# Performance work log

Measured on AMD Instinct MI355X. Metric: run time of the kernel, lower is better.

## Reference

```python
import jax, jax.numpy as jnp
import numpy as np

EPS = 1e-6
NORM_FACTOR = 1000.0  # self.normalization_factor, aggregation 'sum'

# ---- Lorentz manifold (curvature -1, hyperboloid <x,x>_L = -1) ----

def _linner(x, y):
    # Lorentz inner product, keepdim on last axis
    return -x[..., :1] * y[..., :1] + jnp.sum(x[..., 1:] * y[..., 1:], axis=-1, keepdims=True)

def _proj_tan0(u):
    return jnp.concatenate([jnp.zeros_like(u[..., :1]), u[..., 1:]], axis=-1)

def _expmap0(u):
    sp = u[..., 1:]
    n = jnp.sqrt(jnp.clip(jnp.sum(sp * sp, axis=-1, keepdims=True), EPS))
    return jnp.concatenate([jnp.cosh(n), jnp.sinh(n) / n * sp], axis=-1)

def _logmap0(x):
    x0 = jnp.clip(x[..., :1], 1.0 + EPS)
    d = jnp.arccosh(x0)
    sp = x[..., 1:] * (d / jnp.sqrt(x0 * x0 - 1.0))
    return jnp.concatenate([jnp.zeros_like(x0), sp], axis=-1)

def _dist(x, y):
    return jnp.arccosh(jnp.clip(-_linner(x, y), 1.0 + EPS))

def _logmap(x, y):
    alpha = jnp.clip(-_linner(x, y), 1.0 + EPS)
    u = y - alpha * x                      # y + <x,y>_L x
    return jnp.arccosh(alpha) * u / jnp.sqrt(alpha * alpha - 1.0)

def _expmap(x, u):
    n = jnp.sqrt(jnp.clip(_linner(u, u), EPS))
    return jnp.cosh(n) * x + jnp.sinh(n) / n * u

def _proju(x, u):
    return u + _linner(x, u) * x

def _transp0(y, v):
    # parallel transport from origin o=(1,0,...,0) to y
    coef = _linner(y, v) / (1.0 + y[..., :1])
    oy = jnp.concatenate([y[..., :1] + 1.0, y[..., 1:]], axis=-1)
    return v + coef * oy

def _layernorm(x, g, b, eps=1e-5):
    m = jnp.mean(x, axis=-1, keepdims=True)
    v = jnp.mean((x - m) ** 2, axis=-1, keepdims=True)
    return (x - m) / jnp.sqrt(v + eps) * g + b


def setup_inputs() -> dict:
    N, E, D, ED = 10000, 320000, 128, 2
    key = jax.random.key(0)
    ks = jax.random.split(key, 10)
    # nodes on the hyperboloid: expmap0 of a small tangent vector
    h_tan = 0.02 * jax.random.normal(ks[0], (N, D), dtype=jnp.float32)
    h = _expmap0(_proj_tan0(h_tan))
    edge_attr = jax.random.normal(ks[1], (E, ED), dtype=jnp.float32)
    row = jax.random.randint(ks[2], (E,), 0, N, dtype=jnp.int32)
    col = jax.random.randint(ks[3], (E,), 0, N, dtype=jnp.int32)
    node_mask = jnp.ones((N, 1), dtype=jnp.float32)
    edge_mask = jnp.ones((E, 1), dtype=jnp.float32)
    s = 1.0 / np.sqrt(D)
    W = s * jax.random.normal(ks[4], (D, D), dtype=jnp.float32)
    bias = 0.0 * jax.random.normal(ks[5], (1, D), dtype=jnp.float32)  # init.constant_(bias, 0)
    att_in = 2 * D + ED + 1  # x_row, x_col, edge_attr + geodesic
    att_w1 = (1.0 / np.sqrt(att_in)) * jax.random.normal(ks[6], (att_in, D), dtype=jnp.float32)
    att_b1 = jnp.zeros((D,), dtype=jnp.float32)
    att_w2 = s * jax.random.normal(ks[7], (D, 1), dtype=jnp.float32)
    att_b2 = jnp.zeros((1,), dtype=jnp.float32)
    ln_gamma = jnp.ones((D - 1,), dtype=jnp.float32)
    ln_beta = jnp.zeros((D - 1,), dtype=jnp.float32)
    return {"h": h, "edge_attr": edge_attr, "row": row, "col": col,
            "node_mask": node_mask, "edge_mask": edge_mask, "W": W, "bias": bias,
            "att_w1": att_w1, "att_b1": att_b1, "att_w2": att_w2, "att_b2": att_b2,
            "ln_gamma": ln_gamma, "ln_beta": ln_beta}


def reference(h, edge_attr, row, col, node_mask, edge_mask, W, bias,
              att_w1, att_b1, att_w2, att_b2, ln_gamma, ln_beta):
    N = h.shape[0]
    # ---- HypLinear ----
    xt = _logmap0(h) @ W                  # Linear(in,out,bias=False)
    x = _expmap0(_proj_tan0(xt))
    b = _transp0(x, _proj_tan0(bias))
    x = _expmap(x, b)
    # ---- HypAgg ----
    x_tan = _logmap0(x)
    xr, xc = x[row], x[col]
    geo = _dist(xr, xc)                   # [E,1]
    att_in = jnp.concatenate([x_tan[row], x_tan[col], edge_attr, geo], axis=-1)
    hid = jax.nn.silu(att_in @ att_w1 + att_b1)
    att = jax.nn.sigmoid(hid @ att_w2 + att_b2) * edge_mask   # [E,1]
    loc = _logmap(xr, xc)                 # [E,D]
    agg = jax.ops.segment_sum(loc * att, row, num_segments=N) / NORM_FACTOR
    x = _expmap(x, _proju(x, agg))
    # ---- HNorm (Lorentz: LN on spatial components only) ----
    ht = _logmap0(x)
    sp = _layernorm(ht[..., 1:], ln_gamma, ln_beta)
    x = _expmap0(jnp.concatenate([ht[..., :1], sp], axis=-1))
    # ---- HypAct (manifold_out = Lorentz as well) ----
    xt = _proj_tan0(jax.nn.silu(_logmap0(x)))
    return _expmap0(xt)
```

## Files before the change

### kernel.cpp

```cpp
#include <hip/hip_runtime.h>
#include <math.h>

#define D 128
#define NPB 8
#define EPS1 (1.0f + 1e-6f)

__device__ __forceinline__ float dpp_rsum16(float v) {
    v += __int_as_float(__builtin_amdgcn_update_dpp(
        0, __float_as_int(v), 0x121, 0xf, 0xf, true));
    v += __int_as_float(__builtin_amdgcn_update_dpp(
        0, __float_as_int(v), 0x122, 0xf, 0xf, true));
    v += __int_as_float(__builtin_amdgcn_update_dpp(
        0, __float_as_int(v), 0x124, 0xf, 0xf, true));
    v += __int_as_float(__builtin_amdgcn_update_dpp(
        0, __float_as_int(v), 0x128, 0xf, 0xf, true));
    return v;
}

__device__ __forceinline__ float facosh(float a) {
    return __logf(a + sqrtf(fmaxf(a * a - 1.0f, 0.0f)));
}

__device__ __forceinline__ void unpack8(const float4& a, const float4& b,
                                        float* d) {
    d[0] = a.x; d[1] = a.y; d[2] = a.z; d[3] = a.w;
    d[4] = b.x; d[5] = b.y; d[6] = b.z; d[7] = b.w;
}

__device__ __forceinline__ void bsumH(float* v, float (*wred)[4], int lane,
                                      int wid, int kp) {
    __syncthreads();
#pragma unroll
    for (int o = 32; o; o >>= 1)
#pragma unroll
        for (int nl = 0; nl < 4; nl++) v[nl] += __shfl_xor(v[nl], o, 64);
    if (lane == 0)
#pragma unroll
        for (int nl = 0; nl < 4; nl++) wred[wid][nl] = v[nl];
    __syncthreads();
#pragma unroll
    for (int nl = 0; nl < 4; nl++)
        v[nl] = wred[2 * kp][nl] + wred[2 * kp + 1][nl];
}

__global__ __launch_bounds__(256) void node_pre8(
    const float* __restrict__ h, const float* __restrict__ W,
    const float* __restrict__ bias, const float* __restrict__ att_w1,
    const float* __restrict__ att_b1, float* __restrict__ XQ,
    float* __restrict__ P_out, const int* __restrict__ row,
    int* __restrict__ cnt, int N, int E) {
    int i0 = blockIdx.x * NPB;
    int tid = threadIdx.x;
    int j = tid & 127, kp = tid >> 7;
    int lane = tid & 63, wid = tid >> 6;
    int nbase = kp * 4;
    __shared__ __align__(16) float t8[NPB][D];
    __shared__ float psumP[2][NPB][D];
    __shared__ float psumQ[2][NPB][D];
    __shared__ float wred[4][4];

    float hj[4];
#pragma unroll
    for (int nl = 0; nl < 4; nl++) {
        int gi = i0 + nbase + nl;
        hj[nl] = (gi < N) ? h[(size_t)gi * D + j] : 0.0f;
        t8[nbase + nl][j] = hj[nl];
    }
    __syncthreads();
    float tj[4];
#pragma unroll
    for (int nl = 0; nl < 4; nl++) {
        float h0 = fmaxf(t8[nbase + nl][0], EPS1);
        float fac = facosh(h0) * rsqrtf(h0 * h0 - 1.0f);
        tj[nl] = (j == 0) ? 0.0f : hj[nl] * fac;
    }
    __syncthreads();
#pragma unroll
    for (int nl = 0; nl < 4; nl++) t8[nbase + nl][j] = tj[nl];
    __syncthreads();

    float xtp[NPB];
#pragma unroll
    for (int n = 0; n < NPB; n++) xtp[n] = 0.0f;
    int kbeg = kp * 64;
    for (int k0 = kbeg; k0 < kbeg + 64; k0 += 4) {
        float w0 = W[(k0 + 0) * D + j], w1 = W[(k0 + 1) * D + j];
        float w2 = W[(k0 + 2) * D + j], w3 = W[(k0 + 3) * D + j];
#pragma unroll
        for (int n = 0; n < NPB; n++) {
            float4 tv = *(const float4*)&t8[n][k0];
            xtp[n] = fmaf(tv.x, w0,
                          fmaf(tv.y, w1, fmaf(tv.z, w2, fmaf(tv.w, w3, xtp[n]))));
        }
    }
#pragma unroll
    for (int n = 0; n < NPB; n++) psumP[kp][n][j] = xtp[n];
    __syncthreads();
    float xt[4];
#pragma unroll
    for (int nl = 0; nl < 4; nl++) {
        int n = nbase + nl;
        xt[nl] = (j == 0) ? 0.0f : (psumP[0][n][j] + psumP[1][n][j]);
    }

    float v4[4];
#pragma unroll
    for (int nl = 0; nl < 4; nl++) v4[nl] = xt[nl] * xt[nl];
    bsumH(v4, wred, lane, wid, kp);
    float xj[4];
#pragma unroll
    for (int nl = 0; nl < 4; nl++) {
        float nn = sqrtf(fmaxf(v4[nl], 1e-6f));
        float e = __expf(nn), ei = __fdividef(1.0f, e);
        float ch = 0.5f * (e + ei), sh = 0.5f * (e - ei);
        xj[nl] = (j == 0) ? ch : __fdividef(sh, nn) * xt[nl];
    }

    float vj = (j == 0) ? 0.0f : bias[j];
#pragma unroll
    for (int nl = 0; nl < 4; nl++) v4[nl] = xj[nl] * vj;
    bsumH(v4, wred, lane, wid, kp);
    __syncthreads();
#pragma unroll
    for (int nl = 0; nl < 4; nl++) t8[nbase + nl][j] = xj[nl];
    __syncthreads();
    float bj[4];
#pragma unroll
    for (int nl = 0; nl < 4; nl++) {
        float X0 = t8[nbase + nl][0];
        float coef = __fdividef(v4[nl], 1.0f + X0);
        bj[nl] = vj + coef * ((j == 0) ? (X0 + 1.0f) : xj[nl]);
    }
#pragma unroll
    for (int nl = 0; nl < 4; nl++)
        v4[nl] = (j == 0) ? -bj[nl] * bj[nl] : bj[nl] * bj[nl];
    bsumH(v4, wred, lane, wid, kp);
    float xnj[4];
#pragma unroll
    for (int nl = 0; nl < 4; nl++) {
        float nb = sqrtf(fmaxf(v4[nl], 1e-6f));
        float e = __expf(nb), ei = __fdividef(1.0f, e);
        float ch = 0.5f * (e + ei), sh = 0.5f * (e - ei);
        xnj[nl] = ch * xj[nl] + __fdividef(sh, nb) * bj[nl];
        int gi = i0 + nbase + nl;
        if (gi < N) XQ[(size_t)gi * 256 + j] = xnj[nl];
    }

    __syncthreads();
#pragma unroll
    for (int nl = 0; nl < 4; nl++) t8[nbase + nl][j] = xnj[nl];
    __syncthreads();
    float xtj[4];
#pragma unroll
    for (int nl = 0; nl < 4; nl++) {
        float Y0 = fmaxf(t8[nbase + nl][0], EPS1);
        float f = facosh(Y0) * rsqrtf(Y0 * Y0 - 1.0f);
        xtj[nl] = (j == 0) ? 0.0f : xnj[nl] * f;
    }
    __syncthreads();
#pragma unroll
    for (int nl = 0; nl < 4; nl++) t8[nbase + nl][j] = xtj[nl];
    __syncthreads();

    float pp[NPB], qq[NPB];
#pragma unroll
    for (int n = 0; n < NPB; n++) {
        pp[n] = 0.0f;
        qq[n] = 0.0f;
    }
    for (int k0 = kbeg; k0 < kbeg + 64; k0 += 4) {
        float a0 = att_w1[(k0 + 0) * D + j], a1 = att_w1[(k0 + 1) * D + j];
        float a2 = att_w1[(k0 + 2) * D + j], a3 = att_w1[(k0 + 3) * D + j];
        float c0 = att_w1[(D + k0 + 0) * D + j], c1 = att_w1[(D + k0 + 1) * D + j];
        float c2 = att_w1[(D + k0 + 2) * D + j], c3 = att_w1[(D + k0 + 3) * D + j];
#pragma unroll
        for (int n = 0; n < NPB; n++) {
            float4 tv = *(const float4*)&t8[n][k0];
            pp[n] = fmaf(tv.x, a0,
                         fmaf(tv.y, a1, fmaf(tv.z, a2, fmaf(tv.w, a3, pp[n]))));
            qq[n] = fmaf(tv.x, c0,
                         fmaf(tv.y, c1, fmaf(tv.z, c2, fmaf(tv.w, c3, qq[n]))));
        }
    }
#pragma unroll
    for (int n = 0; n < NPB; n++) {
        psumP[kp][n][j] = pp[n];
        psumQ[kp][n][j] = qq[n];
    }
    __syncthreads();
    float b1 = att_b1[j];
#pragma unroll
    for (int nl = 0; nl < 4; nl++) {
        int n = nbase + nl;
        int gi = i0 + n;
        if (gi < N) {
            P_out[(size_t)gi * D + j] = psumP[0][n][j] + psumP[1][n][j] + b1;
            XQ[(size_t)gi * 256 + 128 + j] = psumQ[0][n][j] + psumQ[1][n][j];
        }
    }

    int gtid = blockIdx.x * 256 + tid;
    int tot = gridDim.x * 256;
    for (int e2 = gtid; e2 < E; e2 += tot) atomicAdd(&cnt[row[e2]], 1);
}

__global__ __launch_bounds__(1024) void scan_kernel(const int* __restrict__ cnt,
                                                    int* __restrict__ off,
                                                    int* __restrict__ cursor,
                                                    int N) {
    __shared__ int wsum[16];
    __shared__ int carry_s;
    int tid = threadIdx.x, lane = tid & 63, wid = tid >> 6;
    if (tid == 0) carry_s = 0;
    __syncthreads();
    for (int base = 0; base < N; base += 1024) {
        int idx = base + tid;
        int v = (idx < N) ? cnt[idx] : 0;
        int orig = v;
#pragma unroll
        for (int o = 1; o < 64; o <<= 1) {
            int t = __shfl_up(v, o, 64);
            if (lane >= o) v += t;
        }
        if (lane == 63) wsum[wid] = v;
        __syncthreads();
        if (wid == 0 && lane < 16) {
            int w = wsum[lane];
#pragma unroll
            for (int o = 1; o < 16; o <<= 1) {
                int t = __shfl_up(w, o, 64);
                if (lane >= o) w += t;
            }
            wsum[lane] = w;
        }
        __syncthreads();
        int carry = carry_s;
        int wbase = (wid == 0) ? 0 : wsum[wid - 1];
        int excl = carry + wbase + v - orig;
        if (idx < N) {
            off[idx] = excl;
            cursor[idx] = excl;
        }
        __syncthreads();
        if (tid == 1023) carry_s = carry + wsum[15];
        __syncthreads();
    }
}

__global__ void scatter_kernel(const int* __restrict__ row,
                               const int* __restrict__ col,
                               const float* __restrict__ edge_attr,
                               const float* __restrict__ edge_mask,
                               int* __restrict__ cursor,
                               float4* __restrict__ rec, int E) {
    const float2* ea2 = (const float2*)edge_attr;
    for (int e = blockIdx.x * blockDim.x + threadIdx.x; e < E;
         e += gridDim.x * blockDim.x) {
        int r = row[e];
        int pos = atomicAdd(&cursor[r], 1);
        float2 a = ea2[e];
        rec[pos] = make_float4(__int_as_float(col[e]), a.x, a.y, edge_mask[e]);
    }
}

__global__ __launch_bounds__(256) void edge_agg(
    const float* __restrict__ XQ, const float* __restrict__ P,
    const float4* __restrict__ rec, const int* __restrict__ off,
    const int* __restrict__ cnt, const float* __restrict__ w1c,
    const float* __restrict__ att_w2, const float* __restrict__ att_b2,
    const float* __restrict__ gamma, const float* __restrict__ beta,
    float* __restrict__ out, int N) {
    int tid = threadIdx.x, lane = tid & 63;
    int sub = lane & 15, grp = lane >> 4;
    int i = blockIdx.x * 4 + (tid >> 6);
    bool valid = i < N;
    i = min(i, N - 1);
    int j8 = sub * 8, f4 = sub * 2;

    const float4* w4 = (const float4*)w1c;
    const float4* aw4 = (const float4*)att_w2;
    const float4* xq4r = (const float4*)(XQ + (size_t)i * 256);
    const float4* pr4 = (const float4*)(P + (size_t)i * D);
    float xr[8], pr[8], wa[8], wb[8], wg[8], w2v[8];
    unpack8(xq4r[f4], xq4r[f4 + 1], xr);
    unpack8(pr4[f4], pr4[f4 + 1], pr);
    unpack8(w4[f4], w4[f4 + 1], wa);
    unpack8(w4[32 + f4], w4[32 + f4 + 1], wb);
    unpack8(w4[64 + f4], w4[64 + f4 + 1], wg);
    unpack8(aw4[f4], aw4[f4 + 1], w2v);
    float b2 = att_b2[0];
    float xr0s = (sub == 0) ? -xr[0] : xr[0];

    float acc[8];
#pragma unroll
    for (int u = 0; u < 8; u++) acc[u] = 0.0f;

    int s = off[i], m = valid ? cnt[i] : 0;
    int clen = (m + 3) >> 2;
    int k0 = grp * clen;
    int len = min(m, k0 + clen) - k0;

    auto compute = [&](const float4& rc, const float4& g0, const float4& g1,
                       const float4& g2, const float4& g3, bool act) {
        float xc[8], qc[8];
        unpack8(g0, g1, xc);
        unpack8(g2, g3, qc);
        float lin = xr0s * xc[0];
#pragma unroll
        for (int u = 1; u < 8; u++) lin = fmaf(xr[u], xc[u], lin);
        lin = dpp_rsum16(lin);
        float alpha = fmaxf(-lin, EPS1);
        float a2m = fmaxf(fmaf(alpha, alpha, -1.0f), 1e-12f);
        float rden = rsqrtf(a2m);
        float geo = __logf(fmaf(a2m, rden, alpha));
        float lp = 0.0f;
#pragma unroll
        for (int u = 0; u < 8; u++) {
            float hv = pr[u] + qc[u] +
                       fmaf(rc.y, wa[u], fmaf(rc.z, wb[u], geo * wg[u]));
            float sig = __fdividef(1.0f, 1.0f + __expf(-hv));
            lp = fmaf(hv * sig, w2v[u], lp);
        }
        lp = dpp_rsum16(lp);
        float w = act ? rc.w : 0.0f;
        float att = w * __fdividef(1.0f, 1.0f + __expf(-(lp + b2)));
        float scale = att * geo * rden * 1e-3f;
#pragma unroll
        for (int u = 0; u < 8; u++)
            acc[u] = fmaf(scale, fmaf(-alpha, xr[u], xc[u]), acc[u]);
    };

    float4 rcA = make_float4(__int_as_float(0), 0.0f, 0.0f, 0.0f), rcB;
    if (len > 0) rcA = rec[s + k0];
    const float4* pA =
        (const float4*)(XQ + (size_t)__float_as_int(rcA.x) * 256);
    float4 gA0 = pA[f4], gA1 = pA[f4 + 1], gA2 = pA[32 + f4],
           gA3 = pA[32 + f4 + 1];
    float4 gB0, gB1, gB2, gB3;

    for (int t = 0; t < clen; t += 2) {
        rcB = rcA;
        if (t + 1 < len) rcB = rec[s + k0 + t + 1];
        const float4* pB =
            (const float4*)(XQ + (size_t)__float_as_int(rcB.x) * 256);
        gB0 = pB[f4]; gB1 = pB[f4 + 1]; gB2 = pB[32 + f4]; gB3 = pB[32 + f4 + 1];
        compute(rcA, gA0, gA1, gA2, gA3, t < len);
        rcA = rcB;
        if (t + 2 < len) rcA = rec[s + k0 + t + 2];
        const float4* pN =
            (const float4*)(XQ + (size_t)__float_as_int(rcA.x) * 256);
        gA0 = pN[f4]; gA1 = pN[f4 + 1]; gA2 = pN[32 + f4]; gA3 = pN[32 + f4 + 1];
        compute(rcB, gB0, gB1, gB2, gB3, t + 1 < len);
    }

#pragma unroll
    for (int u = 0; u < 8; u++) {
        acc[u] += __shfl_xor(acc[u], 16, 64);
        acc[u] += __shfl_xor(acc[u], 32, 64);
    }

    float lxa_p = (sub == 0) ? -xr[0] * acc[0] : xr[0] * acc[0];
#pragma unroll
    for (int u = 1; u < 8; u++) lxa_p = fmaf(xr[u], acc[u], lxa_p);
    float lxa = dpp_rsum16(lxa_p);
    float uj[8];
#pragma unroll
    for (int u = 0; u < 8; u++) uj[u] = fmaf(lxa, xr[u], acc[u]);
    float luu_p = (sub == 0) ? -uj[0] * uj[0] : uj[0] * uj[0];
#pragma unroll
    for (int u = 1; u < 8; u++) luu_p = fmaf(uj[u], uj[u], luu_p);
    float luu = dpp_rsum16(luu_p);
    float nn = sqrtf(fmaxf(luu, 1e-6f));
    float e = __expf(nn), ei = __fdividef(1.0f, e);
    float ch = 0.5f * (e + ei), shv = __fdividef(0.5f * (e - ei), nn);
    float xn[8];
#pragma unroll
    for (int u = 0; u < 8; u++) xn[u] = ch * xr[u] + shv * uj[u];
    float X0 = __shfl(xn[0], lane & 48, 64);
    X0 = fmaxf(X0, EPS1);
    float fc = facosh(X0) * rsqrtf(X0 * X0 - 1.0f);
    float ht[8];
#pragma unroll
    for (int u = 0; u < 8; u++) ht[u] = xn[u] * fc;
    if (sub == 0) ht[0] = 0.0f;
    float mp = 0.0f;
#pragma unroll
    for (int u = 0; u < 8; u++) mp += ht[u];
    float mean = dpp_rsum16(mp) * (1.0f / 127.0f);
    float diff[8];
#pragma unroll
    for (int u = 0; u < 8; u++) diff[u] = ht[u] - mean;
    if (sub == 0) diff[0] = 0.0f;
    float vp = 0.0f;
#pragma unroll
    for (int u = 0; u < 8; u++) vp = fmaf(diff[u], diff[u], vp);
    float var = dpp_rsum16(vp) * (1.0f / 127.0f);
    float rstd = rsqrtf(var + 1e-5f);
    float sp[8];
#pragma unroll
    for (int u = 0; u < 8; u++) {
        int j = j8 + u;
        sp[u] = (j > 0) ? fmaf(diff[u] * rstd, gamma[j - 1], beta[j - 1]) : 0.0f;
    }
    float n2p = 0.0f;
#pragma unroll
    for (int u = 0; u < 8; u++) n2p = fmaf(sp[u], sp[u], n2p);
    float n2 = sqrtf(fmaxf(dpp_rsum16(n2p), 1e-6f));
    e = __expf(n2);
    ei = __fdividef(1.0f, e);
    float y0 = 0.5f * (e + ei), sh2 = __fdividef(0.5f * (e - ei), n2);
    float yj[8];
#pragma unroll
    for (int u = 0; u < 8; u++) yj[u] = sh2 * sp[u];
    if (sub == 0) yj[0] = y0;
    float y0c = fmaxf(y0, EPS1);
    float f3 = facosh(y0c) * rsqrtf(y0c * y0c - 1.0f);
    float sj[8];
#pragma unroll
    for (int u = 0; u < 8; u++) {
        float lj = yj[u] * f3;
        sj[u] = __fdividef(lj, 1.0f + __expf(-lj));
    }
    if (sub == 0) sj[0] = 0.0f;
    float n3p = 0.0f;
#pragma unroll
    for (int u = 0; u < 8; u++) n3p = fmaf(sj[u], sj[u], n3p);
    float n3 = sqrtf(fmaxf(dpp_rsum16(n3p), 1e-6f));
    e = __expf(n3);
    ei = __fdividef(1.0f, e);
    float o0 = 0.5f * (e + ei), sh3 = __fdividef(0.5f * (e - ei), n3);
    float ov[8];
#pragma unroll
    for (int u = 0; u < 8; u++) ov[u] = sh3 * sj[u];
    if (sub == 0) ov[0] = o0;
    if (valid && grp == 0) {
        float4* o4 = (float4*)(out + (size_t)i * D);
        o4[f4] = make_float4(ov[0], ov[1], ov[2], ov[3]);
        o4[f4 + 1] = make_float4(ov[4], ov[5], ov[6], ov[7]);
    }
}

extern "C" void kernel_launch(void* const* d_in, const int* in_sizes, int n_in,
                              void* d_out, int out_size, void* d_ws,
                              size_t ws_size, hipStream_t stream) {
    const float* h = (const float*)d_in[0];
    const float* edge_attr = (const float*)d_in[1];
    const int* row = (const int*)d_in[2];
    const int* col = (const int*)d_in[3];
    const float* edge_mask = (const float*)d_in[5];
    const float* W = (const float*)d_in[6];
    const float* bias = (const float*)d_in[7];
    const float* att_w1 = (const float*)d_in[8];
    const float* att_b1 = (const float*)d_in[9];
    const float* att_w2 = (const float*)d_in[10];
    const float* att_b2 = (const float*)d_in[11];
    const float* ln_g = (const float*)d_in[12];
    const float* ln_b = (const float*)d_in[13];

    int N = in_sizes[0] / D;
    int E = in_sizes[2];

    float* XQ = (float*)d_ws;
    float* Pbuf = XQ + (size_t)N * 256;
    float4* rec = (float4*)(Pbuf + (size_t)N * D);
    int* cnt = (int*)(rec + E);
    int* off = cnt + N;
    int* cur = off + N;

    hipMemsetAsync(cnt, 0, N * sizeof(int), stream);
    node_pre8<<<(N + NPB - 1) / NPB, 256, 0, stream>>>(
        h, W, bias, att_w1, att_b1, XQ, Pbuf, row, cnt, N, E);
    scan_kernel<<<1, 1024, 0, stream>>>(cnt, off, cur, N);
    scatter_kernel<<<640, 256, 0, stream>>>(row, col, edge_attr, edge_mask,
                                            cur, rec, E);
    edge_agg<<<(N + 3) / 4, 256, 0, stream>>>(XQ, Pbuf, rec, off, cnt,
                                              att_w1 + 256 * D, att_w2, att_b2,
                                              ln_g, ln_b, (float*)d_out, N);
}
```

Before: 146.4 us.

## Use persistent atomic work-queue in edge_agg and 512-thread node_pre8

edge_agg becomes a persistent kernel with a fixed grid in which each wavefront pulls node indices from a global atomic counter, so degree imbalance is smoothed and LayerNorm gamma/beta loads are hoisted out of the per-node path. node_pre8 moves to 512 threads, splitting the K dimension four ways with 2 nodes per k-slice instead of 4, which gives more waves per block and shorter dependent chains. The trade-offs are an extra memset and one atomic per node, plus more shared-memory partial sums and a four-way reduction in the pre kernel.

```diff
diff --git a/kernel.cpp b/kernel.cpp
--- a/kernel.cpp
+++ b/kernel.cpp
@@ -27,23 +27,23 @@
     d[4] = b.x; d[5] = b.y; d[6] = b.z; d[7] = b.w;
 }
 
-__device__ __forceinline__ void bsumH(float* v, float (*wred)[4], int lane,
-                                      int wid, int kp) {
+__device__ __forceinline__ void bsumH2(float* v, float (*wred)[2], int lane,
+                                       int wid, int kp) {
     __syncthreads();
 #pragma unroll
     for (int o = 32; o; o >>= 1)
 #pragma unroll
-        for (int nl = 0; nl < 4; nl++) v[nl] += __shfl_xor(v[nl], o, 64);
+        for (int nl = 0; nl < 2; nl++) v[nl] += __shfl_xor(v[nl], o, 64);
     if (lane == 0)
 #pragma unroll
-        for (int nl = 0; nl < 4; nl++) wred[wid][nl] = v[nl];
-    __syncthreads();
-#pragma unroll
-    for (int nl = 0; nl < 4; nl++)
+        for (int nl = 0; nl < 2; nl++) wred[wid][nl] = v[nl];
+    __syncthreads();
+#pragma unroll
+    for (int nl = 0; nl < 2; nl++)
         v[nl] = wred[2 * kp][nl] + wred[2 * kp + 1][nl];
 }
 
-__global__ __launch_bounds__(256) void node_pre8(
+__global__ __launch_bounds__(512) void node_pre8(
     const float* __restrict__ h, const float* __restrict__ W,
     const float* __restrict__ bias, const float* __restrict__ att_w1,
     const float* __restrict__ att_b1, float* __restrict__ XQ,
@@ -53,37 +53,37 @@
     int tid = threadIdx.x;
     int j = tid & 127, kp = tid >> 7;
     int lane = tid & 63, wid = tid >> 6;
-    int nbase = kp * 4;
+    int nbase = kp * 2;
     __shared__ __align__(16) float t8[NPB][D];
-    __shared__ float psumP[2][NPB][D];
-    __shared__ float psumQ[2][NPB][D];
-    __shared__ float wred[4][4];
-
-    float hj[4];
-#pragma unroll
-    for (int nl = 0; nl < 4; nl++) {
+    __shared__ float psumP[4][NPB][D];
+    __shared__ float psumQ[4][NPB][D];
+    __shared__ float wred[8][2];
+
+    float hj[2];
+#pragma unroll
+    for (int nl = 0; nl < 2; nl++) {
         int gi = i0 + nbase + nl;
         hj[nl] = (gi < N) ? h[(size_t)gi * D + j] : 0.0f;
         t8[nbase + nl][j] = hj[nl];
     }
     __syncthreads();
-    float tj[4];
-#pragma unroll
-    for (int nl = 0; nl < 4; nl++) {
+    float tj[2];
+#pragma unroll
+    for (int nl = 0; nl < 2; nl++) {
         float h0 = fmaxf(t8[nbase + nl][0], EPS1);
         float fac = facosh(h0) * rsqrtf(h0 * h0 - 1.0f);
         tj[nl] = (j == 0) ? 0.0f : hj[nl] * fac;
     }
     __syncthreads();
 #pragma unroll
-    for (int nl = 0; nl < 4; nl++) t8[nbase + nl][j] = tj[nl];
+    for (int nl = 0; nl < 2; nl++) t8[nbase + nl][j] = tj[nl];
     __syncthreads();
 
     float xtp[NPB];
 #pragma unroll
     for (int n = 0; n < NPB; n++) xtp[n] = 0.0f;
-    int kbeg = kp * 64;
-    for (int k0 = kbeg; k0 < kbeg + 64; k0 += 4) {
+    int kbeg = kp * 32;
+    for (int k0 = kbeg; k0 < kbeg + 32; k0 += 4) {
         float w0 = W[(k0 + 0) * D + j], w1 = W[(k0 + 1) * D + j];
         float w2 = W[(k0 + 2) * D + j], w3 = W[(k0 + 3) * D + j];
 #pragma unroll
@@ -96,21 +96,23 @@
 #pragma unroll
     for (int n = 0; n < NPB; n++) psumP[kp][n][j] = xtp[n];
     __syncthreads();
-    float xt[4];
-#pragma unroll
-    for (int nl = 0; nl < 4; nl++) {
+    float xt[2];
+#pragma unroll
+    for (int nl = 0; nl < 2; nl++) {
         int n = nbase + nl;
-        xt[nl] = (j == 0) ? 0.0f : (psumP[0][n][j] + psumP[1][n][j]);
-    }
-
-    float v4[4];
-#pragma unroll
-    for (int nl = 0; nl < 4; nl++) v4[nl] = xt[nl] * xt[nl];
-    bsumH(v4, wred, lane, wid, kp);
-    float xj[4];
-#pragma unroll
-    for (int nl = 0; nl < 4; nl++) {
-        float nn = sqrtf(fmaxf(v4[nl], 1e-6f));
+        xt[nl] = (j == 0) ? 0.0f
+                          : (psumP[0][n][j] + psumP[1][n][j] + psumP[2][n][j] +
+                             psumP[3][n][j]);
+    }
+
+    float v2[2];
+#pragma unroll
+    for (int nl = 0; nl < 2; nl++) v2[nl] = xt[nl] * xt[nl];
+    bsumH2(v2, wred, lane, wid, kp);
+    float xj[2];
+#pragma unroll
+    for (int nl = 0; nl < 2; nl++) {
+        float nn = sqrtf(fmaxf(v2[nl], 1e-6f));
         float e = __expf(nn), ei = __fdividef(1.0f, e);
         float ch = 0.5f * (e + ei), sh = 0.5f * (e - ei);
         xj[nl] = (j == 0) ? ch : __fdividef(sh, nn) * xt[nl];
@@ -118,27 +120,27 @@
 
     float vj = (j == 0) ? 0.0f : bias[j];
 #pragma unroll
-    for (int nl = 0; nl < 4; nl++) v4[nl] = xj[nl] * vj;
-    bsumH(v4, wred, lane, wid, kp);
-    __syncthreads();
-#pragma unroll
-    for (int nl = 0; nl < 4; nl++) t8[nbase + nl][j] = xj[nl];
-    __syncthreads();
-    float bj[4];
-#pragma unroll
-    for (int nl = 0; nl < 4; nl++) {
+    for (int nl = 0; nl < 2; nl++) v2[nl] = xj[nl] * vj;
+    bsumH2(v2, wred, lane, wid, kp);
+    __syncthreads();
+#pragma unroll
+    for (int nl = 0; nl < 2; nl++) t8[nbase + nl][j] = xj[nl];
+    __syncthreads();
+    float bj[2];
+#pragma unroll
+    for (int nl = 0; nl < 2; nl++) {
         float X0 = t8[nbase + nl][0];
-        float coef = __fdividef(v4[nl], 1.0f + X0);
+        float coef = __fdividef(v2[nl], 1.0f + X0);
         bj[nl] = vj + coef * ((j == 0) ? (X0 + 1.0f) : xj[nl]);
     }
 #pragma unroll
-    for (int nl = 0; nl < 4; nl++)
-        v4[nl] = (j == 0) ? -bj[nl] * bj[nl] : bj[nl] * bj[nl];
-    bsumH(v4, wred, lane, wid, kp);
-    float xnj[4];
-#pragma unroll
-    for (int nl = 0; nl < 4; nl++) {
-        float nb = sqrtf(fmaxf(v4[nl], 1e-6f));
+    for (int nl = 0; nl < 2; nl++)
+        v2[nl] = (j == 0) ? -bj[nl] * bj[nl] : bj[nl] * bj[nl];
+    bsumH2(v2, wred, lane, wid, kp);
+    float xnj[2];
+#pragma unroll
+    for (int nl = 0; nl < 2; nl++) {
+        float nb = sqrtf(fmaxf(v2[nl], 1e-6f));
         float e = __expf(nb), ei = __fdividef(1.0f, e);
         float ch = 0.5f * (e + ei), sh = 0.5f * (e - ei);
         xnj[nl] = ch * xj[nl] + __fdividef(sh, nb) * bj[nl];
@@ -148,18 +150,18 @@
 
     __syncthreads();
 #pragma unroll
-    for (int nl = 0; nl < 4; nl++) t8[nbase + nl][j] = xnj[nl];
-    __syncthreads();
-    float xtj[4];
-#pragma unroll
-    for (int nl = 0; nl < 4; nl++) {
+    for (int nl = 0; nl < 2; nl++) t8[nbase + nl][j] = xnj[nl];
+    __syncthreads();
+    float xtj[2];
+#pragma unroll
+    for (int nl = 0; nl < 2; nl++) {
         float Y0 = fmaxf(t8[nbase + nl][0], EPS1);
         float f = facosh(Y0) * rsqrtf(Y0 * Y0 - 1.0f);
         xtj[nl] = (j == 0) ? 0.0f : xnj[nl] * f;
     }
     __syncthreads();
 #pragma unroll
-    for (int nl = 0; nl < 4; nl++) t8[nbase + nl][j] = xtj[nl];
+    for (int nl = 0; nl < 2; nl++) t8[nbase + nl][j] = xtj[nl];
     __syncthreads();
 
     float pp[NPB], qq[NPB];
@@ -168,7 +170,7 @@
         pp[n] = 0.0f;
         qq[n] = 0.0f;
     }
-    for (int k0 = kbeg; k0 < kbeg + 64; k0 += 4) {
+    for (int k0 = kbeg; k0 < kbeg + 32; k0 += 4) {
         float a0 = att_w1[(k0 + 0) * D + j], a1 = att_w1[(k0 + 1) * D + j];
         float a2 = att_w1[(k0 + 2) * D + j], a3 = att_w1[(k0 + 3) * D + j];
         float c0 = att_w1[(D + k0 + 0) * D + j], c1 = att_w1[(D + k0 + 1) * D + j];
@@ -190,17 +192,19 @@
     __syncthreads();
     float b1 = att_b1[j];
 #pragma unroll
-    for (int nl = 0; nl < 4; nl++) {
+    for (int nl = 0; nl < 2; nl++) {
         int n = nbase + nl;
         int gi = i0 + n;
         if (gi < N) {
-            P_out[(size_t)gi * D + j] = psumP[0][n][j] + psumP[1][n][j] + b1;
-            XQ[(size_t)gi * 256 + 128 + j] = psumQ[0][n][j] + psumQ[1][n][j];
-        }
-    }
-
-    int gtid = blockIdx.x * 256 + tid;
-    int tot = gridDim.x * 256;
+            P_out[(size_t)gi * D + j] = psumP[0][n][j] + psumP[1][n][j] +
+                                        psumP[2][n][j] + psumP[3][n][j] + b1;
+            XQ[(size_t)gi * 256 + 128 + j] = psumQ[0][n][j] + psumQ[1][n][j] +
+                                             psumQ[2][n][j] + psumQ[3][n][j];
+        }
+    }
+
+    int gtid = blockIdx.x * 512 + tid;
+    int tot = gridDim.x * 512;
     for (int e2 = gtid; e2 < E; e2 += tot) atomicAdd(&cnt[row[e2]], 1);
 }
 
@@ -269,174 +273,188 @@
     const int* __restrict__ cnt, const float* __restrict__ w1c,
     const float* __restrict__ att_w2, const float* __restrict__ att_b2,
     const float* __restrict__ gamma, const float* __restrict__ beta,
-    float* __restrict__ out, int N) {
+    float* __restrict__ out, int* __restrict__ wctr, int N) {
     int tid = threadIdx.x, lane = tid & 63;
     int sub = lane & 15, grp = lane >> 4;
-    int i = blockIdx.x * 4 + (tid >> 6);
-    bool valid = i < N;
-    i = min(i, N - 1);
     int j8 = sub * 8, f4 = sub * 2;
 
     const float4* w4 = (const float4*)w1c;
     const float4* aw4 = (const float4*)att_w2;
-    const float4* xq4r = (const float4*)(XQ + (size_t)i * 256);
-    const float4* pr4 = (const float4*)(P + (size_t)i * D);
-    float xr[8], pr[8], wa[8], wb[8], wg[8], w2v[8];
-    unpack8(xq4r[f4], xq4r[f4 + 1], xr);
-    unpack8(pr4[f4], pr4[f4 + 1], pr);
+    float wa[8], wb[8], wg[8], w2v[8];
     unpack8(w4[f4], w4[f4 + 1], wa);
     unpack8(w4[32 + f4], w4[32 + f4 + 1], wb);
     unpack8(w4[64 + f4], w4[64 + f4 + 1], wg);
     unpack8(aw4[f4], aw4[f4 + 1], w2v);
     float b2 = att_b2[0];
-    float xr0s = (sub == 0) ? -xr[0] : xr[0];
-
-    float acc[8];
-#pragma unroll
-    for (int u = 0; u < 8; u++) acc[u] = 0.0f;
-
-    int s = off[i], m = valid ? cnt[i] : 0;
-    int clen = (m + 3) >> 2;
-    int k0 = grp * clen;
-    int len = min(m, k0 + clen) - k0;
-
-    auto compute = [&](const float4& rc, const float4& g0, const float4& g1,
-                       const float4& g2, const float4& g3, bool act) {
-        float xc[8], qc[8];
-        unpack8(g0, g1, xc);
-        unpack8(g2, g3, qc);
-        float lin = xr0s * xc[0];
-#pragma unroll
-        for (int u = 1; u < 8; u++) lin = fmaf(xr[u], xc[u], lin);
-        lin = dpp_rsum16(lin);
-        float alpha = fmaxf(-lin, EPS1);
-        float a2m = fmaxf(fmaf(alpha, alpha, -1.0f), 1e-12f);
-        float rden = rsqrtf(a2m);
-        float geo = __logf(fmaf(a2m, rden, alpha));
-        float lp = 0.0f;
-#pragma unroll
-        for (int u = 0; u < 8; u++) {
-            float hv = pr[u] + qc[u] +
-                       fmaf(rc.y, wa[u], fmaf(rc.z, wb[u], geo * wg[u]));
-            float sig = __fdividef(1.0f, 1.0f + __expf(-hv));
-            lp = fmaf(hv * sig, w2v[u], lp);
-        }
-        lp = dpp_rsum16(lp);
-        float w = act ? rc.w : 0.0f;
-        float att = w * __fdividef(1.0f, 1.0f + __expf(-(lp + b2)));
-        float scale = att * geo * rden * 1e-3f;
-#pragma unroll
-        for (int u = 0; u < 8; u++)
-            acc[u] = fmaf(scale, fmaf(-alpha, xr[u], xc[u]), acc[u]);
-    };
-
-    float4 rcA = make_float4(__int_as_float(0), 0.0f, 0.0f, 0.0f), rcB;
-    if (len > 0) rcA = rec[s + k0];
-    const float4* pA =
-        (const float4*)(XQ + (size_t)__float_as_int(rcA.x) * 256);
-    float4 gA0 = pA[f4], gA1 = pA[f4 + 1], gA2 = pA[32 + f4],
-           gA3 = pA[32 + f4 + 1];
-    float4 gB0, gB1, gB2, gB3;
-
-    for (int t = 0; t < clen; t += 2) {
-        rcB = rcA;
-        if (t + 1 < len) rcB = rec[s + k0 + t + 1];
-        const float4* pB =
-            (const float4*)(XQ + (size_t)__float_as_int(rcB.x) * 256);
-        gB0 = pB[f4]; gB1 = pB[f4 + 1]; gB2 = pB[32 + f4]; gB3 = pB[32 + f4 + 1];
-        compute(rcA, gA0, gA1, gA2, gA3, t < len);
-        rcA = rcB;
-        if (t + 2 < len) rcA = rec[s + k0 + t + 2];
-        const float4* pN =
-            (const float4*)(XQ + (size_t)__float_as_int(rcA.x) * 256);
-        gA0 = pN[f4]; gA1 = pN[f4 + 1]; gA2 = pN[32 + f4]; gA3 = pN[32 + f4 + 1];
-        compute(rcB, gB0, gB1, gB2, gB3, t + 1 < len);
-    }
-
-#pragma unroll
-    for (int u = 0; u < 8; u++) {
-        acc[u] += __shfl_xor(acc[u], 16, 64);
-        acc[u] += __shfl_xor(acc[u], 32, 64);
-    }
-
-    float lxa_p = (sub == 0) ? -xr[0] * acc[0] : xr[0] * acc[0];
-#pragma unroll
-    for (int u = 1; u < 8; u++) lxa_p = fmaf(xr[u], acc[u], lxa_p);
-    float lxa = dpp_rsum16(lxa_p);
-    float uj[8];
-#pragma unroll
-    for (int u = 0; u < 8; u++) uj[u] = fmaf(lxa, xr[u], acc[u]);
-    float luu_p = (sub == 0) ? -uj[0] * uj[0] : uj[0] * uj[0];
-#pragma unroll
-    for (int u = 1; u < 8; u++) luu_p = fmaf(uj[u], uj[u], luu_p);
-    float luu = dpp_rsum16(luu_p);
-    float nn = sqrtf(fmaxf(luu, 1e-6f));
-    float e = __expf(nn), ei = __fdividef(1.0f, e);
-    float ch = 0.5f * (e + ei), shv = __fdividef(0.5f * (e - ei), nn);
-    float xn[8];
-#pragma unroll
-    for (int u = 0; u < 8; u++) xn[u] = ch * xr[u] + shv * uj[u];
-    float X0 = __shfl(xn[0], lane & 48, 64);
-    X0 = fmaxf(X0, EPS1);
-    float fc = facosh(X0) * rsqrtf(X0 * X0 - 1.0f);
-    float ht[8];
-#pragma unroll
-    for (int u = 0; u < 8; u++) ht[u] = xn[u] * fc;
-    if (sub == 0) ht[0] = 0.0f;
-    float mp = 0.0f;
-#pragma unroll
-    for (int u = 0; u < 8; u++) mp += ht[u];
-    float mean = dpp_rsum16(mp) * (1.0f / 127.0f);
-    float diff[8];
-#pragma unroll
-    for (int u = 0; u < 8; u++) diff[u] = ht[u] - mean;
-    if (sub == 0) diff[0] = 0.0f;
-    float vp = 0.0f;
-#pragma unroll
-    for (int u = 0; u < 8; u++) vp = fmaf(diff[u], diff[u], vp);
-    float var = dpp_rsum16(vp) * (1.0f / 127.0f);
-    float rstd = rsqrtf(var + 1e-5f);
-    float sp[8];
+    float g_ln[8], bt_ln[8];
 #pragma unroll
     for (int u = 0; u < 8; u++) {
         int j = j8 + u;
-        sp[u] = (j > 0) ? fmaf(diff[u] * rstd, gamma[j - 1], beta[j - 1]) : 0.0f;
-    }
-    float n2p = 0.0f;
-#pragma unroll
-    for (int u = 0; u < 8; u++) n2p = fmaf(sp[u], sp[u], n2p);
-    float n2 = sqrtf(fmaxf(dpp_rsum16(n2p), 1e-6f));
-    e = __expf(n2);
-    ei = __fdividef(1.0f, e);
-    float y0 = 0.5f * (e + ei), sh2 = __fdividef(0.5f * (e - ei), n2);
-    float yj[8];
-#pragma unroll
-    for (int u = 0; u < 8; u++) yj[u] = sh2 * sp[u];
-    if (sub == 0) yj[0] = y0;
-    float y0c = fmaxf(y0, EPS1);
-    float f3 = facosh(y0c) * rsqrtf(y0c * y0c - 1.0f);
-    float sj[8];
-#pragma unroll
-    for (int u = 0; u < 8; u++) {
-        float lj = yj[u] * f3;
-        sj[u] = __fdividef(lj, 1.0f + __expf(-lj));
-    }
-    if (sub == 0) sj[0] = 0.0f;
-    float n3p = 0.0f;
-#pragma unroll
-    for (int u = 0; u < 8; u++) n3p = fmaf(sj[u], sj[u], n3p);
-    float n3 = sqrtf(fmaxf(dpp_rsum16(n3p), 1e-6f));
-    e = __expf(n3);
-    ei = __fdividef(1.0f, e);
-    float o0 = 0.5f * (e + ei), sh3 = __fdividef(0.5f * (e - ei), n3);
-    float ov[8];
-#pragma unroll
-    for (int u = 0; u < 8; u++) ov[u] = sh3 * sj[u];
-    if (sub == 0) ov[0] = o0;
-    if (valid && grp == 0) {
-        float4* o4 = (float4*)(out + (size_t)i * D);
-        o4[f4] = make_float4(ov[0], ov[1], ov[2], ov[3]);
-        o4[f4 + 1] = make_float4(ov[4], ov[5], ov[6], ov[7]);
+        g_ln[u] = (j > 0) ? gamma[j - 1] : 0.0f;
+        bt_ln[u] = (j > 0) ? beta[j - 1] : 0.0f;
+    }
+
+    for (;;) {
+        int ipop;
+        if (lane == 0) ipop = atomicAdd(wctr, 1);
+        int i = __builtin_amdgcn_readfirstlane(ipop);
+        if (i >= N) break;
+
+        const float4* xq4r = (const float4*)(XQ + (size_t)i * 256);
+        const float4* pr4 = (const float4*)(P + (size_t)i * D);
+        float xr[8], pr[8];
+        unpack8(xq4r[f4], xq4r[f4 + 1], xr);
+        unpack8(pr4[f4], pr4[f4 + 1], pr);
+        float xr0s = (sub == 0) ? -xr[0] : xr[0];
+
+        float acc[8];
+#pragma unroll
+        for (int u = 0; u < 8; u++) acc[u] = 0.0f;
+
+        int s = off[i], m = cnt[i];
+        int clen = (m + 3) >> 2;
+        int k0 = grp * clen;
+        int len = min(m, k0 + clen) - k0;
+
+        auto compute = [&](const float4& rc, const float4& g0, const float4& g1,
+                           const float4& g2, const float4& g3, bool act) {
+            float xc[8], qc[8];
+            unpack8(g0, g1, xc);
+            unpack8(g2, g3, qc);
+            float lin = xr0s * xc[0];
+#pragma unroll
+            for (int u = 1; u < 8; u++) lin = fmaf(xr[u], xc[u], lin);
+            lin = dpp_rsum16(lin);
+            float alpha = fmaxf(-lin, EPS1);
+            float a2m = fmaxf(fmaf(alpha, alpha, -1.0f), 1e-12f);
+            float rden = rsqrtf(a2m);
+            float geo = __logf(fmaf(a2m, rden, alpha));
+            float lp = 0.0f;
+#pragma unroll
+            for (int u = 0; u < 8; u++) {
+                float hv = pr[u] + qc[u] +
+                           fmaf(rc.y, wa[u], fmaf(rc.z, wb[u], geo * wg[u]));
+                float sig = __fdividef(1.0f, 1.0f + __expf(-hv));
+                lp = fmaf(hv * sig, w2v[u], lp);
+            }
+            lp = dpp_rsum16(lp);
+            float w = act ? rc.w : 0.0f;
+            float att = w * __fdividef(1.0f, 1.0f + __expf(-(lp + b2)));
+            float scale = att * geo * rden * 1e-3f;
+#pragma unroll
+            for (int u = 0; u < 8; u++)
+                acc[u] = fmaf(scale, fmaf(-alpha, xr[u], xc[u]), acc[u]);
+        };
+
+        float4 rcA = make_float4(__int_as_float(0), 0.0f, 0.0f, 0.0f), rcB;
+        if (len > 0) rcA = rec[s + k0];
+        const float4* pA =
+            (const float4*)(XQ + (size_t)__float_as_int(rcA.x) * 256);
+        float4 gA0 = pA[f4], gA1 = pA[f4 + 1], gA2 = pA[32 + f4],
+               gA3 = pA[32 + f4 + 1];
+        float4 gB0, gB1, gB2, gB3;
+
+        for (int t = 0; t < clen; t += 2) {
+            rcB = rcA;
+            if (t + 1 < len) rcB = rec[s + k0 + t + 1];
+            const float4* pB =
+                (const float4*)(XQ + (size_t)__float_as_int(rcB.x) * 256);
+            gB0 = pB[f4]; gB1 = pB[f4 + 1]; gB2 = pB[32 + f4];
+            gB3 = pB[32 + f4 + 1];
+            compute(rcA, gA0, gA1, gA2, gA3, t < len);
+            rcA = rcB;
+            if (t + 2 < len) rcA = rec[s + k0 + t + 2];
+            const float4* pN =
+                (const float4*)(XQ + (size_t)__float_as_int(rcA.x) * 256);
+            gA0 = pN[f4]; gA1 = pN[f4 + 1]; gA2 = pN[32 + f4];
+            gA3 = pN[32 + f4 + 1];
+            compute(rcB, gB0, gB1, gB2, gB3, t + 1 < len);
+        }
+
+#pragma unroll
+        for (int u = 0; u < 8; u++) {
+            acc[u] += __shfl_xor(acc[u], 16, 64);
+            acc[u] += __shfl_xor(acc[u], 32, 64);
+        }
+
+        float lxa_p = (sub == 0) ? -xr[0] * acc[0] : xr[0] * acc[0];
+#pragma unroll
+        for (int u = 1; u < 8; u++) lxa_p = fmaf(xr[u], acc[u], lxa_p);
+        float lxa = dpp_rsum16(lxa_p);
+        float uj[8];
+#pragma unroll
+        for (int u = 0; u < 8; u++) uj[u] = fmaf(lxa, xr[u], acc[u]);
+        float luu_p = (sub == 0) ? -uj[0] * uj[0] : uj[0] * uj[0];
+#pragma unroll
+        for (int u = 1; u < 8; u++) luu_p = fmaf(uj[u], uj[u], luu_p);
+        float luu = dpp_rsum16(luu_p);
+        float nn = sqrtf(fmaxf(luu, 1e-6f));
+        float e = __expf(nn), ei = __fdividef(1.0f, e);
+        float ch = 0.5f * (e + ei), shv = __fdividef(0.5f * (e - ei), nn);
+        float xn[8];
+#pragma unroll
+        for (int u = 0; u < 8; u++) xn[u] = ch * xr[u] + shv * uj[u];
+        float X0 = __shfl(xn[0], lane & 48, 64);
+        X0 = fmaxf(X0, EPS1);
+        float fc = facosh(X0) * rsqrtf(X0 * X0 - 1.0f);
+        float ht[8];
+#pragma unroll
+        for (int u = 0; u < 8; u++) ht[u] = xn[u] * fc;
+        if (sub == 0) ht[0] = 0.0f;
+        float mp = 0.0f;
+#pragma unroll
+        for (int u = 0; u < 8; u++) mp += ht[u];
+        float mean = dpp_rsum16(mp) * (1.0f / 127.0f);
+        float diff[8];
+#pragma unroll
+        for (int u = 0; u < 8; u++) diff[u] = ht[u] - mean;
+        if (sub == 0) diff[0] = 0.0f;
+        float vp = 0.0f;
+#pragma unroll
+        for (int u = 0; u < 8; u++) vp = fmaf(diff[u], diff[u], vp);
+        float var = dpp_rsum16(vp) * (1.0f / 127.0f);
+        float rstd = rsqrtf(var + 1e-5f);
+        float sp[8];
+#pragma unroll
+        for (int u = 0; u < 8; u++)
+            sp[u] = fmaf(diff[u] * rstd, g_ln[u], bt_ln[u]);
+        if (sub == 0) sp[0] = 0.0f;
+        float n2p = 0.0f;
+#pragma unroll
+        for (int u = 0; u < 8; u++) n2p = fmaf(sp[u], sp[u], n2p);
+        float n2 = sqrtf(fmaxf(dpp_rsum16(n2p), 1e-6f));
+        e = __expf(n2);
+        ei = __fdividef(1.0f, e);
+        float y0 = 0.5f * (e + ei), sh2 = __fdividef(0.5f * (e - ei), n2);
+        float yj[8];
+#pragma unroll
+        for (int u = 0; u < 8; u++) yj[u] = sh2 * sp[u];
+        if (sub == 0) yj[0] = y0;
+        float y0c = fmaxf(y0, EPS1);
+        float f3 = facosh(y0c) * rsqrtf(y0c * y0c - 1.0f);
+        float sj[8];
+#pragma unroll
+        for (int u = 0; u < 8; u++) {
+            float lj = yj[u] * f3;
+            sj[u] = __fdividef(lj, 1.0f + __expf(-lj));
+        }
+        if (sub == 0) sj[0] = 0.0f;
+        float n3p = 0.0f;
+#pragma unroll
+        for (int u = 0; u < 8; u++) n3p = fmaf(sj[u], sj[u], n3p);
+        float n3 = sqrtf(fmaxf(dpp_rsum16(n3p), 1e-6f));
+        e = __expf(n3);
+        ei = __fdividef(1.0f, e);
+        float o0 = 0.5f * (e + ei), sh3 = __fdividef(0.5f * (e - ei), n3);
+        float ov[8];
+#pragma unroll
+        for (int u = 0; u < 8; u++) ov[u] = sh3 * sj[u];
+        if (sub == 0) ov[0] = o0;
+        if (grp == 0) {
+            float4* o4 = (float4*)(out + (size_t)i * D);
+            o4[f4] = make_float4(ov[0], ov[1], ov[2], ov[3]);
+            o4[f4 + 1] = make_float4(ov[4], ov[5], ov[6], ov[7]);
+        }
     }
 }
 
@@ -466,14 +484,16 @@
     int* cnt = (int*)(rec + E);
     int* off = cnt + N;
     int* cur = off + N;
+    int* wctr = cur + N;
 
     hipMemsetAsync(cnt, 0, N * sizeof(int), stream);
-    node_pre8<<<(N + NPB - 1) / NPB, 256, 0, stream>>>(
+    hipMemsetAsync(wctr, 0, sizeof(int), stream);
+    node_pre8<<<(N + NPB - 1) / NPB, 512, 0, stream>>>(
         h, W, bias, att_w1, att_b1, XQ, Pbuf, row, cnt, N, E);
     scan_kernel<<<1, 1024, 0, stream>>>(cnt, off, cur, N);
     scatter_kernel<<<640, 256, 0, stream>>>(row, col, edge_attr, edge_mask,
                                             cur, rec, E);
-    edge_agg<<<(N + 3) / 4, 256, 0, stream>>>(XQ, Pbuf, rec, off, cnt,
-                                              att_w1 + 256 * D, att_w2, att_b2,
-                                              ln_g, ln_b, (float*)d_out, N);
-}
+    edge_agg<<<2048, 256, 0, stream>>>(XQ, Pbuf, rec, off, cnt,
+                                       att_w1 + 256 * D, att_w2, att_b2, ln_g,
+                                       ln_b, (float*)d_out, wctr, N);
+}
```

After: 313.0 us. 2.14x slower.
